# Kernel tuning notes

Hardware: AMD Instinct MI355X
Metric: run time of the kernel (lower is better)

## Reference

```python
import jax, jax.numpy as jnp
import numpy as np

B, L, E, H, EXP = 2, 2048, 1024, 16, 4
D = E // H
EPS = 1e-5

def layernorm(x, g, b):
    mu = jnp.mean(x, axis=-1, keepdims=True)
    var = jnp.var(x, axis=-1, keepdims=True)
    return (x - mu) * jax.lax.rsqrt(var + EPS) * g + b

def setup_inputs() -> dict:
    key = jax.random.key(0)
    ks = jax.random.split(key, 12)
    s = 0.02
    return {
        "x": jax.random.normal(ks[0], (B, L, E), dtype=jnp.float32),
        "ln1_g": jnp.ones((E,), jnp.float32),
        "ln1_b": jnp.zeros((E,), jnp.float32),
        "W_qkv": jax.random.normal(ks[1], (E, 3 * E), dtype=jnp.float32) * s,
        "W_proj": jax.random.normal(ks[2], (E, E), dtype=jnp.float32) * s,
        "b_proj": jnp.zeros((E,), jnp.float32),
        "ln2_g": jnp.ones((E,), jnp.float32),
        "ln2_b": jnp.zeros((E,), jnp.float32),
        "W1": jax.random.normal(ks[3], (E, EXP * E), dtype=jnp.float32) * s,
        "b1": jnp.zeros((EXP * E,), jnp.float32),
        "W2": jax.random.normal(ks[4], (EXP * E, E), dtype=jnp.float32) * s,
        "b2": jnp.zeros((E,), jnp.float32),
    }

def reference(x, ln1_g, ln1_b, W_qkv, W_proj, b_proj, ln2_g, ln2_b, W1, b1, W2, b2):
    # --- attention sub-block (pre-LN) ---
    h = layernorm(x, ln1_g, ln1_b)                      # [B,L,E]
    qkv = h @ W_qkv                                      # [B,L,3E]
    q, k, v = jnp.split(qkv, 3, axis=-1)
    q = q.reshape(B, L, H, D).transpose(0, 2, 1, 3)      # [B,H,L,D]
    k = k.reshape(B, L, H, D).transpose(0, 2, 1, 3)
    v = v.reshape(B, L, H, D).transpose(0, 2, 1, 3)
    scale = jnp.sqrt(jnp.float32(E))                     # NOTE: module divides by sqrt(E), not sqrt(D)
    att = jnp.einsum('bhqd,bhkd->bhqk', q, k) / scale
    att = jax.nn.softmax(att, axis=-1)
    out = jnp.einsum('bhqk,bhkd->bhqd', att, v)          # [B,H,L,D]
    out = out.transpose(0, 2, 1, 3).reshape(B, L, E)
    x = x + out @ W_proj + b_proj                         # residual
    # --- feed-forward sub-block (pre-LN) ---
    h = layernorm(x, ln2_g, ln2_b)
    h = jax.nn.gelu(h @ W1 + b1, approximate=False)       # torch GELU is exact erf
    x = x + h @ W2 + b2
    return x
```

## Files before the change

kernel.cpp:

```cpp
#include <hip/hip_runtime.h>
#include <cstdint>
#include <cstddef>


typedef __bf16 bht;
typedef __attribute__((ext_vector_type(8))) __bf16 bf16x8;
typedef __attribute__((ext_vector_type(4))) __bf16 bf16x4;
typedef __attribute__((ext_vector_type(4))) float f32x4;
typedef __attribute__((ext_vector_type(4))) short short4v;

#define B_ 2
#define L_ 2048
#define E_ 1024
#define H_ 16
#define D_ 64
#define ROWS_ (B_ * L_)

#define QSCALE_ 0.045084441f

__device__ __forceinline__ void glds16(const void* g, void* l) {
    __builtin_amdgcn_global_load_lds(
        (const __attribute__((address_space(1))) unsigned int*)g,
        (__attribute__((address_space(3))) unsigned int*)l, 16, 0, 0);
}

__device__ __forceinline__ short4v as_s4(bf16x4 v) {
    return __builtin_bit_cast(short4v, v);
}

__global__ __launch_bounds__(256)
void transpose_cast(const float* __restrict__ in, bht* __restrict__ out, int R, int C) {
    __shared__ float tile[32][33];
    const int bx = blockIdx.x * 32;
    const int by = blockIdx.y * 32;
    const int tx = threadIdx.x, ty = threadIdx.y;
    #pragma unroll
    for (int i = 0; i < 32; i += 8)
        tile[ty + i][tx] = in[(size_t)(by + ty + i) * C + bx + tx];
    __syncthreads();
    #pragma unroll
    for (int i = 0; i < 32; i += 8)
        out[(size_t)(bx + ty + i) * R + by + tx] = (bht)tile[tx][ty + i];
}

__global__ __launch_bounds__(256)
void ln_kernel(const float* __restrict__ x, const float* __restrict__ g,
               const float* __restrict__ b, bht* __restrict__ out) {
    const int row = blockIdx.x, t = threadIdx.x;
    const float4 v = ((const float4*)(x + (size_t)row * E_))[t];
    float s  = v.x + v.y + v.z + v.w;
    float ss = v.x*v.x + v.y*v.y + v.z*v.z + v.w*v.w;
    #pragma unroll
    for (int off = 32; off > 0; off >>= 1) {
        s  += __shfl_down(s, off);
        ss += __shfl_down(ss, off);
    }
    __shared__ float red[8];
    const int wave = t >> 6, lane = t & 63;
    if (lane == 0) { red[wave] = s; red[4 + wave] = ss; }
    __syncthreads();
    s  = red[0] + red[1] + red[2] + red[3];
    ss = red[4] + red[5] + red[6] + red[7];
    const float mean = s * (1.0f / (float)E_);
    const float var  = ss * (1.0f / (float)E_) - mean * mean;
    const float rstd = rsqrtf(var + 1e-5f);
    const float4 gv = ((const float4*)g)[t];
    const float4 bv = ((const float4*)b)[t];
    bf16x4 o;
    o.x = (bht)((v.x - mean) * rstd * gv.x + bv.x);
    o.y = (bht)((v.y - mean) * rstd * gv.y + bv.y);
    o.z = (bht)((v.z - mean) * rstd * gv.z + bv.z);
    o.w = (bht)((v.w - mean) * rstd * gv.w + bv.w);
    *(bf16x4*)(out + (size_t)row * E_ + t * 4) = o;
}

enum { EPI_QKV = 0, EPI_RESID = 1, EPI_GELU = 2 };

template <int EPI>
__global__ __launch_bounds__(256)
void gemm_bt(const bht* __restrict__ A, const bht* __restrict__ Bt,
             const float* __restrict__ bias, const float* __restrict__ resid,
             void* __restrict__ outp,
             bht* __restrict__ qo, bht* __restrict__ ko, bht* __restrict__ vto,
             int M, int N, int K) {
    __shared__ __align__(16) char smem[33792];
    bht* As = (bht*)smem;
    bht* Bs = (bht*)(smem + 16384);
    const int t = threadIdx.x;
    const int lane = t & 63, wave = t >> 6;
    const int lane15 = lane & 15, quad = lane >> 4;
    const int waveM = wave >> 1, waveN = wave & 1;
    const int bm = blockIdx.y * 128, bn = blockIdx.x * 128;

    f32x4 acc[4][4];
    #pragma unroll
    for (int i = 0; i < 4; ++i)
        #pragma unroll
        for (int j = 0; j < 4; ++j)
            acc[i][j] = f32x4{0.f, 0.f, 0.f, 0.f};

    const int swz = lane15 & 7;

    for (int k0 = 0; k0 < K; k0 += 64) {
        #pragma unroll
        for (int i = 0; i < 4; ++i) {
            const int g = i * 256 + t;
            const int row = g >> 3;
            const int col = ((g & 7) ^ (row & 7)) * 8;
            glds16(A  + (size_t)(bm + row) * K + k0 + col, (char*)As + (size_t)g * 16);
            glds16(Bt + (size_t)(bn + row) * K + k0 + col, (char*)Bs + (size_t)g * 16);
        }
        __syncthreads();
        #pragma unroll
        for (int kk = 0; kk < 2; ++kk) {
            const int pc = ((kk * 4 + quad) ^ swz) * 8;
            bf16x8 af[4], bfv[4];
            #pragma unroll
            for (int i = 0; i < 4; ++i)
                af[i] = *(const bf16x8*)(As + (waveM * 64 + i * 16 + lane15) * 64 + pc);
            #pragma unroll
            for (int j = 0; j < 4; ++j)
                bfv[j] = *(const bf16x8*)(Bs + (waveN * 64 + j * 16 + lane15) * 64 + pc);
            #pragma unroll
            for (int i = 0; i < 4; ++i)
                #pragma unroll
                for (int j = 0; j < 4; ++j)
                    acc[i][j] = __builtin_amdgcn_mfma_f32_16x16x32_bf16(af[i], bfv[j], acc[i][j], 0, 0, 0);
        }
        __syncthreads();
    }

    if constexpr (EPI == EPI_QKV) {
        if (bn >= 2048) {
            bht* Vtile = (bht*)smem;
            #pragma unroll
            for (int i = 0; i < 4; ++i) {
                const int rl0 = waveM * 64 + i * 16 + quad * 4;
                #pragma unroll
                for (int j = 0; j < 4; ++j) {
                    const int cl = waveN * 64 + j * 16 + lane15;
                    #pragma unroll
                    for (int r = 0; r < 4; ++r)
                        Vtile[(size_t)cl * 132 + rl0 + r] = (bht)acc[i][j][r];
                }
            }
            __syncthreads();
            const int b = bm >> 11;
            const int l0 = bm & 2047;
            #pragma unroll
            for (int it = 0; it < 8; ++it) {
                const int row = it * 16 + (t >> 4);
                const int ch  = t & 15;
                const int cg = (bn - 2048) + row;
                const int h = cg >> 6, d = cg & 63;
                const int bh = b * H_ + h;
                *(bf16x8*)(vto + ((size_t)bh * D_ + d) * L_ + l0 + ch * 8) =
                    *(const bf16x8*)(Vtile + (size_t)row * 132 + ch * 8);
            }
        } else {
            #pragma unroll
            for (int i = 0; i < 4; ++i) {
                const int row0 = bm + waveM * 64 + i * 16 + quad * 4;
                #pragma unroll
                for (int j = 0; j < 4; ++j) {
                    const int col = bn + waveN * 64 + j * 16 + lane15;
                    const int seg = col >> 10;
                    const int c = col & 1023;
                    const int h = c >> 6, d = c & 63;
                    #pragma unroll
                    for (int r = 0; r < 4; ++r) {
                        const int m = row0 + r;
                        const int b = m >> 11, l = m & 2047;
                        const int bh = b * H_ + h;
                        const float v = acc[i][j][r];
                        if (seg == 0)
                            qo[((size_t)bh * L_ + l) * D_ + d] = (bht)(v * QSCALE_);
                        else
                            ko[((size_t)bh * L_ + l) * D_ + d] = (bht)v;
                    }
                }
            }
        }
    } else {
        #pragma unroll
        for (int i = 0; i < 4; ++i) {
            const int row0 = bm + waveM * 64 + i * 16 + quad * 4;
            #pragma unroll
            for (int j = 0; j < 4; ++j) {
                const int col = bn + waveN * 64 + j * 16 + lane15;
                #pragma unroll
                for (int r = 0; r < 4; ++r) {
                    const int m = row0 + r;
                    float v = acc[i][j][r];
                    if (EPI == EPI_RESID) {
                        ((float*)outp)[(size_t)m * N + col] =
                            v + bias[col] + resid[(size_t)m * N + col];
                    } else {
                        v += bias[col];
                        v = 0.5f * v * (1.0f + erff(v * 0.70710678118654752f));
                        ((bht*)outp)[(size_t)m * N + col] = (bht)v;
                    }
                }
            }
        }
    }
}

template <int EPI>
__global__ __launch_bounds__(256)
void gemm_bt64(const bht* __restrict__ A, const bht* __restrict__ Bt,
               const float* __restrict__ bias, const float* __restrict__ resid,
               void* __restrict__ outp, int M, int N, int K) {
    __shared__ __align__(16) bht As[64 * 64];
    __shared__ __align__(16) bht Bs[128 * 64];
    const int t = threadIdx.x;
    const int lane = t & 63, wave = t >> 6;
    const int lane15 = lane & 15, quad = lane >> 4;
    const int waveM = wave >> 1, waveN = wave & 1;
    const int bm = blockIdx.y * 64, bn = blockIdx.x * 128;

    f32x4 acc[2][4];
    #pragma unroll
    for (int i = 0; i < 2; ++i)
        #pragma unroll
        for (int j = 0; j < 4; ++j)
            acc[i][j] = f32x4{0.f, 0.f, 0.f, 0.f};

    const int swz = lane15 & 7;

    for (int k0 = 0; k0 < K; k0 += 64) {
        #pragma unroll
        for (int i = 0; i < 2; ++i) {
            const int g = i * 256 + t;
            const int row = g >> 3;
            const int col = ((g & 7) ^ (row & 7)) * 8;
            glds16(A + (size_t)(bm + row) * K + k0 + col, (char*)As + (size_t)g * 16);
        }
        #pragma unroll
        for (int i = 0; i < 4; ++i) {
            const int g = i * 256 + t;
            const int row = g >> 3;
            const int col = ((g & 7) ^ (row & 7)) * 8;
            glds16(Bt + (size_t)(bn + row) * K + k0 + col, (char*)Bs + (size_t)g * 16);
        }
        __syncthreads();
        #pragma unroll
        for (int kk = 0; kk < 2; ++kk) {
            const int pc = ((kk * 4 + quad) ^ swz) * 8;
            bf16x8 af[2], bfv[4];
            #pragma unroll
            for (int i = 0; i < 2; ++i)
                af[i] = *(const bf16x8*)(As + (waveM * 32 + i * 16 + lane15) * 64 + pc);
            #pragma unroll
            for (int j = 0; j < 4; ++j)
                bfv[j] = *(const bf16x8*)(Bs + (waveN * 64 + j * 16 + lane15) * 64 + pc);
            #pragma unroll
            for (int i = 0; i < 2; ++i)
                #pragma unroll
                for (int j = 0; j < 4; ++j)
                    acc[i][j] = __builtin_amdgcn_mfma_f32_16x16x32_bf16(af[i], bfv[j], acc[i][j], 0, 0, 0);
        }
        __syncthreads();
    }

    #pragma unroll
    for (int i = 0; i < 2; ++i) {
        const int row0 = bm + waveM * 32 + i * 16 + quad * 4;
        #pragma unroll
        for (int j = 0; j < 4; ++j) {
            const int col = bn + waveN * 64 + j * 16 + lane15;
            #pragma unroll
            for (int r = 0; r < 4; ++r) {
                const int m = row0 + r;
                float v = acc[i][j][r];
                if (EPI == EPI_RESID) {
                    ((float*)outp)[(size_t)m * N + col] =
                        v + bias[col] + resid[(size_t)m * N + col];
                } else {
                    v += bias[col];
                    v = 0.5f * v * (1.0f + erff(v * 0.70710678118654752f));
                    ((bht*)outp)[(size_t)m * N + col] = (bht)v;
                }
            }
        }
    }
}

#define KT_ 128

__global__ __launch_bounds__(256)
void attn_kernel(const bht* __restrict__ Q, const bht* __restrict__ Kb,
                 const bht* __restrict__ Vt, bht* __restrict__ O) {
    __shared__ __align__(16) bht Ks[KT_ * 64];
    __shared__ __align__(16) bht Vs[64 * KT_];
    __shared__ float Ls[4][16];
    const int t = threadIdx.x;
    const int lane = t & 63, wave = t >> 6;
    const int lane15 = lane & 15, quad = lane >> 4;
    const int bh = blockIdx.x, qt = blockIdx.y;

    const bht* Qh = Q  + (size_t)bh * L_ * D_;
    const bht* Kh = Kb + (size_t)bh * L_ * D_;
    const bht* Vh = Vt + (size_t)bh * D_ * L_;

    const int q0 = qt * 64 + wave * 16;

    bf16x8 aq[2];
    #pragma unroll
    for (int kc = 0; kc < 2; ++kc)
        aq[kc] = *(const bf16x8*)(Qh + (size_t)(q0 + lane15) * D_ + kc * 32 + quad * 8);

    f32x4 o_acc[4];
    #pragma unroll
    for (int db = 0; db < 4; ++db) o_acc[db] = f32x4{0.f, 0.f, 0.f, 0.f};
    float l_sum = 0.f;

    const int pc0 = (quad ^ (lane15 & 7)) * 8;
    const int pc1 = pc0 ^ 32;

    for (int kt = 0; kt < L_ / KT_; ++kt) {
        const int key0 = kt * KT_;
        #pragma unroll
        for (int i = 0; i < 4; ++i) {
            const int g = i * 256 + t;
            const int krow = g >> 3;
            const int ksc = ((g & 7) ^ (krow & 7)) * 8;
            glds16(Kh + (size_t)(key0 + krow) * D_ + ksc, (char*)Ks + (size_t)g * 16);
        }
        #pragma unroll
        for (int i = 0; i < 4; ++i) {
            const int g = i * 256 + t;
            const int vrow = g >> 4;
            const int vsc = ((g & 15) ^ (vrow & 7)) * 8;
            glds16(Vh + (size_t)vrow * L_ + key0 + vsc, (char*)Vs + (size_t)g * 16);
        }
        __syncthreads();

        #pragma unroll
        for (int nb = 0; nb < 8; ++nb) {
            const bf16x8 ak0 = *(const bf16x8*)(Ks + (nb * 16 + lane15) * 64 + pc0);
            const bf16x8 ak1 = *(const bf16x8*)(Ks + (nb * 16 + lane15) * 64 + pc1);
            f32x4 st = __builtin_amdgcn_mfma_f32_16x16x32_bf16(
                ak0, aq[0], f32x4{0.f, 0.f, 0.f, 0.f}, 0, 0, 0);
            st = __builtin_amdgcn_mfma_f32_16x16x32_bf16(ak1, aq[1], st, 0, 0, 0);
            bf16x4 pk;
            #pragma unroll
            for (int r = 0; r < 4; ++r) {
                const float pv = exp2f(st[r]);
                l_sum += pv;
                pk[r] = (bht)pv;
            }
            const short4v pf = as_s4(pk);
            #pragma unroll
            for (int db = 0; db < 4; ++db) {
                const int row = db * 16 + lane15;
                const int c16 = (nb * 2 + (quad >> 1)) ^ (row & 7);
                const bf16x4 bv = *(const bf16x4*)(Vs + row * KT_ + c16 * 8 + (quad & 1) * 4);
                o_acc[db] = __builtin_amdgcn_mfma_f32_16x16x16bf16_1k(
                    pf, as_s4(bv), o_acc[db], 0, 0, 0);
            }
        }
        __syncthreads();
    }

    l_sum += __shfl_xor(l_sum, 16);
    l_sum += __shfl_xor(l_sum, 32);
    Ls[wave][lane15] = l_sum;
    asm volatile("s_waitcnt lgkmcnt(0)" ::: "memory");

    const int b = bh >> 4, h = bh & 15;
    #pragma unroll
    for (int r = 0; r < 4; ++r) {
        const int l = q0 + quad * 4 + r;
        const float inv = 1.0f / Ls[wave][quad * 4 + r];
        #pragma unroll
        for (int db = 0; db < 4; ++db)
            O[((size_t)b * L_ + l) * E_ + h * 64 + db * 16 + lane15] =
                (bht)(o_acc[db][r] * inv);
    }
}

extern "C" void kernel_launch(void* const* d_in, const int* in_sizes, int n_in,
                              void* d_out, int out_size, void* d_ws, size_t ws_size,
                              hipStream_t stream) {
    const float* x      = (const float*)d_in[0];
    const float* ln1_g  = (const float*)d_in[1];
    const float* ln1_b  = (const float*)d_in[2];
    const float* W_qkv  = (const float*)d_in[3];
    const float* W_proj = (const float*)d_in[4];
    const float* b_proj = (const float*)d_in[5];
    const float* ln2_g  = (const float*)d_in[6];
    const float* ln2_b  = (const float*)d_in[7];
    const float* W1     = (const float*)d_in[8];
    const float* b1     = (const float*)d_in[9];
    const float* W2     = (const float*)d_in[10];
    const float* b2     = (const float*)d_in[11];
    float* out = (float*)d_out;

    char* ws = (char*)d_ws;
    auto alloc = [&](size_t bytes) {
        char* p = ws;
        ws += (bytes + 255) & ~(size_t)255;
        return p;
    };
    bht*   WqkvT  = (bht*)alloc((size_t)3072 * 1024 * 2);
    bht*   WprojT = (bht*)alloc((size_t)1024 * 1024 * 2);
    bht*   W1T    = (bht*)alloc((size_t)4096 * 1024 * 2);
    bht*   W2T    = (bht*)alloc((size_t)1024 * 4096 * 2);
    bht*   hb     = (bht*)alloc((size_t)ROWS_ * E_ * 2);
    float* x1     = (float*)alloc((size_t)ROWS_ * E_ * 4);
    bht*   Qb     = (bht*)alloc((size_t)B_ * H_ * L_ * D_ * 2);
    bht*   Kbuf   = (bht*)alloc((size_t)B_ * H_ * L_ * D_ * 2);
    bht*   Vtb    = (bht*)alloc((size_t)B_ * H_ * D_ * L_ * 2);
    bht*   attno  = (bht*)alloc((size_t)ROWS_ * E_ * 2);
    bht*   ffn1   = Qb;

    transpose_cast<<<dim3(3072 / 32, 1024 / 32), dim3(32, 8), 0, stream>>>(W_qkv, WqkvT, 1024, 3072);
    transpose_cast<<<dim3(1024 / 32, 1024 / 32), dim3(32, 8), 0, stream>>>(W_proj, WprojT, 1024, 1024);
    transpose_cast<<<dim3(4096 / 32, 1024 / 32), dim3(32, 8), 0, stream>>>(W1, W1T, 1024, 4096);
    transpose_cast<<<dim3(1024 / 32, 4096 / 32), dim3(32, 8), 0, stream>>>(W2, W2T, 4096, 1024);

    ln_kernel<<<ROWS_, 256, 0, stream>>>(x, ln1_g, ln1_b, hb);

    gemm_bt<EPI_QKV><<<dim3(3072 / 128, ROWS_ / 128), 256, 0, stream>>>(
        hb, WqkvT, nullptr, nullptr, nullptr, Qb, Kbuf, Vtb, ROWS_, 3072, 1024);

    attn_kernel<<<dim3(B_ * H_, L_ / 64), 256, 0, stream>>>(Qb, Kbuf, Vtb, attno);

    gemm_bt64<EPI_RESID><<<dim3(1024 / 128, ROWS_ / 64), 256, 0, stream>>>(
        attno, WprojT, b_proj, x, x1, ROWS_, 1024, 1024);

    ln_kernel<<<ROWS_, 256, 0, stream>>>(x1, ln2_g, ln2_b, hb);

    gemm_bt<EPI_GELU><<<dim3(4096 / 128, ROWS_ / 128), 256, 0, stream>>>(
        hb, W1T, b1, nullptr, ffn1, nullptr, nullptr, nullptr, ROWS_, 4096, 1024);

    gemm_bt64<EPI_RESID><<<dim3(1024 / 128, ROWS_ / 64), 256, 0, stream>>>(
        ffn1, W2T, b2, x1, out, ROWS_, 1024, 4096);

    (void)in_sizes; (void)n_in; (void)out_size; (void)ws_size;
}
```

Before: 386.4 us.

## Process two 16-row query sub-tiles per wave in attention kernel

Each wave now handles 32 query rows instead of 16, so every K and V tile loaded into LDS, and every fragment read from it, feeds twice as many MFMAs. The grid's query dimension is halved to match, cutting global/LDS traffic per query. In exchange register pressure roughly doubles for accumulators, and with only 512 blocks occupancy and load balance may suffer. The V swizzle index is rewritten using lane15, which is equivalent to the old row & 7.

```diff
diff --git a/kernel.cpp b/kernel.cpp
--- a/kernel.cpp
+++ b/kernel.cpp
@@ -293,7 +293,7 @@
                  const bht* __restrict__ Vt, bht* __restrict__ O) {
     __shared__ __align__(16) bht Ks[KT_ * 64];
     __shared__ __align__(16) bht Vs[64 * KT_];
-    __shared__ float Ls[4][16];
+    __shared__ float Ls[4][32];
     const int t = threadIdx.x;
     const int lane = t & 63, wave = t >> 6;
     const int lane15 = lane & 15, quad = lane >> 4;
@@ -303,17 +303,23 @@
     const bht* Kh = Kb + (size_t)bh * L_ * D_;
     const bht* Vh = Vt + (size_t)bh * D_ * L_;
 
-    const int q0 = qt * 64 + wave * 16;
-
-    bf16x8 aq[2];
-    #pragma unroll
-    for (int kc = 0; kc < 2; ++kc)
-        aq[kc] = *(const bf16x8*)(Qh + (size_t)(q0 + lane15) * D_ + kc * 32 + quad * 8);
-
-    f32x4 o_acc[4];
-    #pragma unroll
-    for (int db = 0; db < 4; ++db) o_acc[db] = f32x4{0.f, 0.f, 0.f, 0.f};
-    float l_sum = 0.f;
+    const int q0 = qt * 128 + wave * 32;
+
+    bf16x8 aq[2][2];
+    #pragma unroll
+    for (int qs = 0; qs < 2; ++qs)
+        #pragma unroll
+        for (int kc = 0; kc < 2; ++kc)
+            aq[qs][kc] = *(const bf16x8*)(Qh +
+                (size_t)(q0 + qs * 16 + lane15) * D_ + kc * 32 + quad * 8);
+
+    f32x4 o_acc[2][4];
+    #pragma unroll
+    for (int qs = 0; qs < 2; ++qs)
+        #pragma unroll
+        for (int db = 0; db < 4; ++db)
+            o_acc[qs][db] = f32x4{0.f, 0.f, 0.f, 0.f};
+    float l_sum[2] = {0.f, 0.f};
 
     const int pc0 = (quad ^ (lane15 & 7)) * 8;
     const int pc1 = pc0 ^ 32;
@@ -340,44 +346,57 @@
         for (int nb = 0; nb < 8; ++nb) {
             const bf16x8 ak0 = *(const bf16x8*)(Ks + (nb * 16 + lane15) * 64 + pc0);
             const bf16x8 ak1 = *(const bf16x8*)(Ks + (nb * 16 + lane15) * 64 + pc1);
-            f32x4 st = __builtin_amdgcn_mfma_f32_16x16x32_bf16(
-                ak0, aq[0], f32x4{0.f, 0.f, 0.f, 0.f}, 0, 0, 0);
-            st = __builtin_amdgcn_mfma_f32_16x16x32_bf16(ak1, aq[1], st, 0, 0, 0);
-            bf16x4 pk;
-            #pragma unroll
-            for (int r = 0; r < 4; ++r) {
-                const float pv = exp2f(st[r]);
-                l_sum += pv;
-                pk[r] = (bht)pv;
-            }
-            const short4v pf = as_s4(pk);
+            short4v pf[2];
+            #pragma unroll
+            for (int qs = 0; qs < 2; ++qs) {
+                f32x4 st = __builtin_amdgcn_mfma_f32_16x16x32_bf16(
+                    ak0, aq[qs][0], f32x4{0.f, 0.f, 0.f, 0.f}, 0, 0, 0);
+                st = __builtin_amdgcn_mfma_f32_16x16x32_bf16(ak1, aq[qs][1], st, 0, 0, 0);
+                bf16x4 pk;
+                #pragma unroll
+                for (int r = 0; r < 4; ++r) {
+                    const float pv = exp2f(st[r]);
+                    l_sum[qs] += pv;
+                    pk[r] = (bht)pv;
+                }
+                pf[qs] = as_s4(pk);
+            }
             #pragma unroll
             for (int db = 0; db < 4; ++db) {
                 const int row = db * 16 + lane15;
-                const int c16 = (nb * 2 + (quad >> 1)) ^ (row & 7);
+                const int c16 = (nb * 2 + (quad >> 1)) ^ (lane15 & 7);
                 const bf16x4 bv = *(const bf16x4*)(Vs + row * KT_ + c16 * 8 + (quad & 1) * 4);
-                o_acc[db] = __builtin_amdgcn_mfma_f32_16x16x16bf16_1k(
-                    pf, as_s4(bv), o_acc[db], 0, 0, 0);
-            }
-        }
-        __syncthreads();
-    }
-
-    l_sum += __shfl_xor(l_sum, 16);
-    l_sum += __shfl_xor(l_sum, 32);
-    Ls[wave][lane15] = l_sum;
+                const short4v bvs = as_s4(bv);
+                #pragma unroll
+                for (int qs = 0; qs < 2; ++qs)
+                    o_acc[qs][db] = __builtin_amdgcn_mfma_f32_16x16x16bf16_1k(
+                        pf[qs], bvs, o_acc[qs][db], 0, 0, 0);
+            }
+        }
+        __syncthreads();
+    }
+
+    #pragma unroll
+    for (int qs = 0; qs < 2; ++qs) {
+        float s = l_sum[qs];
+        s += __shfl_xor(s, 16);
+        s += __shfl_xor(s, 32);
+        Ls[wave][qs * 16 + lane15] = s;
+    }
     asm volatile("s_waitcnt lgkmcnt(0)" ::: "memory");
 
     const int b = bh >> 4, h = bh & 15;
     #pragma unroll
-    for (int r = 0; r < 4; ++r) {
-        const int l = q0 + quad * 4 + r;
-        const float inv = 1.0f / Ls[wave][quad * 4 + r];
-        #pragma unroll
-        for (int db = 0; db < 4; ++db)
-            O[((size_t)b * L_ + l) * E_ + h * 64 + db * 16 + lane15] =
-                (bht)(o_acc[db][r] * inv);
-    }
+    for (int qs = 0; qs < 2; ++qs)
+        #pragma unroll
+        for (int r = 0; r < 4; ++r) {
+            const int l = q0 + qs * 16 + quad * 4 + r;
+            const float inv = 1.0f / Ls[wave][qs * 16 + quad * 4 + r];
+            #pragma unroll
+            for (int db = 0; db < 4; ++db)
+                O[((size_t)b * L_ + l) * E_ + h * 64 + db * 16 + lane15] =
+                    (bht)(o_acc[qs][db][r] * inv);
+        }
 }
 
 extern "C" void kernel_launch(void* const* d_in, const int* in_sizes, int n_in,
@@ -425,7 +444,7 @@
     gemm_bt<EPI_QKV><<<dim3(3072 / 128, ROWS_ / 128), 256, 0, stream>>>(
         hb, WqkvT, nullptr, nullptr, nullptr, Qb, Kbuf, Vtb, ROWS_, 3072, 1024);
 
-    attn_kernel<<<dim3(B_ * H_, L_ / 64), 256, 0, stream>>>(Qb, Kbuf, Vtb, attno);
+    attn_kernel<<<dim3(B_ * H_, L_ / 128), 256, 0, stream>>>(Qb, Kbuf, Vtb, attno);
 
     gemm_bt64<EPI_RESID><<<dim3(1024 / 128, ROWS_ / 64), 256, 0, stream>>>(
         attno, WprojT, b_proj, x, x1, ROWS_, 1024, 1024);
```

Measured after the change: 396.4 us. +2.6%, slower.
